# Kernel optimization log

Hardware: AMD Instinct MI355X
Metric: run time of the kernel (lower is better)

Reference implementation:

```python
import jax, jax.numpy as jnp
import numpy as np

N_HEAD = 16
NUM_GROUPS = 2


def setup_inputs() -> dict:
    key = jax.random.key(0)
    k1, k2, k3 = jax.random.split(key, 3)
    B, T, D = 4, 2048, 1024
    x = jax.random.normal(k1, (B, T, D), dtype=jnp.float32)
    W_attn = jax.random.normal(k2, (D, 3 * D), dtype=jnp.float32) * 0.02
    b_attn = jnp.zeros((3 * D,), dtype=jnp.float32)
    W_proj = jax.random.normal(k3, (D, D), dtype=jnp.float32) * 0.02
    b_proj = jnp.zeros((D,), dtype=jnp.float32)
    return {"x": x, "W_attn": W_attn, "b_attn": b_attn, "W_proj": W_proj, "b_proj": b_proj}


def _rope_tables(T, d_head):
    # thetas = 1000 ** (-2*arange(1, d/2+1)/d), repeat_interleave(2); positions start at 1
    half = d_head // 2
    thetas = 1000.0 ** (-2.0 * jnp.arange(1, half + 1, dtype=jnp.float32) / d_head)
    thetas = jnp.repeat(thetas, 2)                      # (d_head,)
    pos = jnp.arange(1, T + 1, dtype=jnp.float32)       # (T,)
    args = pos[:, None] * thetas[None, :]               # (T, d_head)
    return jnp.sin(args), jnp.cos(args)


def _apply_rope(x, sin, cos):
    # x: (B, H, T, d_head)
    x_odd = x[..., ::2]
    x_even = x[..., 1::2]
    x_sin = jnp.stack([-x_even, x_odd], axis=-1).reshape(x.shape)  # [-x1, x0, -x3, x2, ...]
    return x * cos + x_sin * sin


def reference(x, W_attn, b_attn, W_proj, b_proj):
    B, T, D = x.shape
    H = N_HEAD
    hd = D // H
    group_dim = D // NUM_GROUPS  # scale divisor; split degenerates to one group since group_dim >= hd

    qkv = x @ W_attn + b_attn                              # (B, T, 3D)
    q, k, v = jnp.split(qkv, 3, axis=-1)

    def split_heads(t):
        return t.reshape(B, T, H, hd).transpose(0, 2, 1, 3)  # (B, H, T, hd)

    q, k, v = split_heads(q), split_heads(k), split_heads(v)

    sin, cos = _rope_tables(T, hd)
    q = _apply_rope(q, sin, cos)
    k = _apply_rope(k, sin, cos)

    # NOTE: original forward never applies the causal mask (attn_mask=None) -> full softmax
    scores = jnp.einsum('bhqd,bhkd->bhqk', q, k) / jnp.sqrt(jnp.float32(group_dim))
    attn = jax.nn.softmax(scores, axis=-1)
    out = jnp.einsum('bhqk,bhkd->bhqd', attn, v)           # (B, H, T, hd)

    out = out.transpose(0, 2, 1, 3).reshape(B, T, D)       # merge heads
    return out @ W_proj + b_proj
```

## Files before the change

kernel.cpp:

```cpp
#include <hip/hip_runtime.h>
#include <hip/hip_bf16.h>
#include <stdint.h>

#define DEVI __device__ __forceinline__

using bf16x8 = __attribute__((ext_vector_type(8))) short;
using f32x4  = __attribute__((ext_vector_type(4))) float;
using f16x4  = __attribute__((ext_vector_type(4))) _Float16;
using f16x8  = __attribute__((ext_vector_type(8))) _Float16;

static constexpr int Bc = 4;
static constexpr int Tc = 2048;
static constexpr int Dc = 1024;
static constexpr int Hc = 16;
static constexpr int HDc = 64;
#define QSCALE 0.06375788883274286f

#if __has_builtin(__builtin_amdgcn_exp2f)
#define EXP2F __builtin_amdgcn_exp2f
#else
#define EXP2F exp2f
#endif

typedef const unsigned int __attribute__((address_space(1)))* gas1_t;
typedef unsigned int __attribute__((address_space(3)))* las3_t;

DEVI void gld16(const void* g, void* l)
{
    __builtin_amdgcn_global_load_lds((gas1_t)(uintptr_t)g, (las3_t)(uintptr_t)l, 16, 0, 0);
}


__global__ void f2bf_kernel(const float4* __restrict__ x, ushort4* __restrict__ y, int n4)
{
    const int base = blockIdx.x * 1024 + threadIdx.x;
#pragma unroll
    for (int u = 0; u < 4; u++) {
        const int i = base + u * 256;
        float4 v = x[i];
        union { __hip_bfloat16 h[4]; ushort4 u4; } cv;
        cv.h[0] = __float2bfloat16(v.x);
        cv.h[1] = __float2bfloat16(v.y);
        cv.h[2] = __float2bfloat16(v.z);
        cv.h[3] = __float2bfloat16(v.w);
        y[i] = cv.u4;
    }
}

__global__ void transpose_bf_kernel(const float* __restrict__ W, __hip_bfloat16* __restrict__ Wt,
                                    int K, int N)
{
    __shared__ float tile[64][65];
    const int n0 = blockIdx.x * 64, k0 = blockIdx.y * 64;
    const int tx = threadIdx.x & 15, ty = threadIdx.x >> 4;
#pragma unroll
    for (int i2 = 0; i2 < 4; i2++) {
        const int k = ty + 16 * i2;
        float4 v = *(const float4*)&W[(size_t)(k0 + k) * N + n0 + tx * 4];
        tile[tx * 4 + 0][k] = v.x;
        tile[tx * 4 + 1][k] = v.y;
        tile[tx * 4 + 2][k] = v.z;
        tile[tx * 4 + 3][k] = v.w;
    }
    __syncthreads();
#pragma unroll
    for (int i2 = 0; i2 < 4; i2++) {
        const int n = ty + 16 * i2;
        union { __hip_bfloat16 h[4]; ushort4 u4; } cv;
#pragma unroll
        for (int c = 0; c < 4; c++)
            cv.h[c] = (__hip_bfloat16)tile[n][tx * 4 + c];
        *(ushort4*)&Wt[(size_t)(n0 + n) * K + k0 + tx * 4] = cv.u4;
    }
}

__global__ void rope_tab_kernel(float* __restrict__ sinT, float* __restrict__ cosT)
{
    int i = blockIdx.x * blockDim.x + threadIdx.x;
    int t = i >> 6, dim = i & 63;
    int p = dim >> 1;
    float theta = powf(1000.f, -2.f * (float)(p + 1) / 64.f);
    float arg = (float)(t + 1) * theta;
    sinT[i] = sinf(arg);
    cosT[i] = cosf(arg);
}


template <int MODE>
__global__ __launch_bounds__(256, 2) void gemm128(
    const __hip_bfloat16* __restrict__ A, const __hip_bfloat16* __restrict__ Bt,
    const float* __restrict__ bias, int M, int N, int K,
    const float* __restrict__ sinT, const float* __restrict__ cosT,
    __hip_bfloat16* __restrict__ Qb, __hip_bfloat16* __restrict__ Kb,
    _Float16* __restrict__ Vb, float* __restrict__ Cout)
{
    __shared__ __align__(16) __hip_bfloat16 sA[2][128 * 64];
    __shared__ __align__(16) __hip_bfloat16 sB[2][128 * 64];
    const int tid = threadIdx.x;
    const int wave = tid >> 6, lane = tid & 63;
    const int qd = lane >> 4, lm = lane & 15;
    const int wm = (wave >> 1) * 64, wn = (wave & 1) * 64;
    const int tileM = blockIdx.y * 128, tileN = blockIdx.x * 128;

    const int srow = tid >> 3;
    const int socc = (tid & 7) ^ (srow & 7);

    f32x4 acc[4][4];
#pragma unroll
    for (int i = 0; i < 4; i++)
#pragma unroll
        for (int j = 0; j < 4; j++)
            acc[i][j] = (f32x4){0.f, 0.f, 0.f, 0.f};

    const __hip_bfloat16* pa = A + (size_t)(tileM + srow) * K + socc * 8;
    const __hip_bfloat16* pb = Bt + (size_t)(tileN + srow) * K + socc * 8;

    auto stageT = [&](int p, int k0) {
#pragma unroll
        for (int it = 0; it < 4; it++) {
            gld16(pa + (size_t)(it * 32) * K + k0, &sA[p][it * 2048 + wave * 512]);
            gld16(pb + (size_t)(it * 32) * K + k0, &sB[p][it * 2048 + wave * 512]);
        }
    };

    stageT(0, 0);

    const int swl = (lm & 7) << 3;
    const int nk = K / 64;
    for (int kt = 0; kt < nk; kt++) {
        const int p = kt & 1;
        if (kt + 1 < nk) {
            stageT(p ^ 1, (kt + 1) * 64);
            __builtin_amdgcn_s_waitcnt(0xF78);
        } else {
            __builtin_amdgcn_s_waitcnt(0xF70);
        }
        __builtin_amdgcn_s_barrier();

#pragma unroll
        for (int ks = 0; ks < 2; ks++) {
            bf16x8 wf[4], xf[4];
#pragma unroll
            for (int a = 0; a < 4; a++)
                wf[a] = *(const bf16x8*)&sB[p][(wn + a * 16 + lm) * 64
                                              + ((ks * 32 + qd * 8) ^ swl)];
#pragma unroll
            for (int b = 0; b < 4; b++)
                xf[b] = *(const bf16x8*)&sA[p][(wm + b * 16 + lm) * 64
                                              + ((ks * 32 + qd * 8) ^ swl)];
#pragma unroll
            for (int a = 0; a < 4; a++)
#pragma unroll
                for (int b = 0; b < 4; b++)
                    acc[a][b] = __builtin_amdgcn_mfma_f32_16x16x32_bf16(
                        wf[a], xf[b], acc[a][b], 0, 0, 0);
        }
        __builtin_amdgcn_s_barrier();
    }

    if constexpr (MODE == 0) {
        const int sec = tileN >> 10;
        const int h = ((tileN + wn) & 1023) >> 6;
#pragma unroll
        for (int a = 0; a < 4; a++) {
            const int dim0 = a * 16 + qd * 4;
            const int n0 = tileN + wn + dim0;
            const float4 bi = *(const float4*)&bias[n0];
#pragma unroll
            for (int b = 0; b < 4; b++) {
                const int m = tileM + wm + b * 16 + lm;
                const int t = m & (Tc - 1), bb = m >> 11;
                const float v0 = acc[a][b][0] + bi.x;
                const float v1 = acc[a][b][1] + bi.y;
                const float v2 = acc[a][b][2] + bi.z;
                const float v3 = acc[a][b][3] + bi.w;
                if (sec < 2) {
                    const float4 sn = *(const float4*)&sinT[t * 64 + dim0];
                    const float4 cs = *(const float4*)&cosT[t * 64 + dim0];
                    const float o0 = v0 * cs.x - v1 * sn.x;
                    const float o1 = v1 * cs.y + v0 * sn.y;
                    const float o2 = v2 * cs.z - v3 * sn.z;
                    const float o3 = v3 * cs.w + v2 * sn.w;
                    union { __hip_bfloat16 hx[4]; ushort4 u4; } cv;
                    if (sec == 0) {
                        cv.hx[0] = (__hip_bfloat16)(o0 * QSCALE);
                        cv.hx[1] = (__hip_bfloat16)(o1 * QSCALE);
                        cv.hx[2] = (__hip_bfloat16)(o2 * QSCALE);
                        cv.hx[3] = (__hip_bfloat16)(o3 * QSCALE);
                        *(ushort4*)&Qb[((size_t)(bb * Hc + h) * Tc + t) * HDc + dim0] = cv.u4;
                    } else {
                        cv.hx[0] = (__hip_bfloat16)o0;
                        cv.hx[1] = (__hip_bfloat16)o1;
                        cv.hx[2] = (__hip_bfloat16)o2;
                        cv.hx[3] = (__hip_bfloat16)o3;
                        const int dswb = dim0 ^ ((t & 7) << 3);
                        *(ushort4*)&Kb[((size_t)(bb * Hc + h) * Tc + t) * HDc + dswb] = cv.u4;
                    }
                } else {
                    const int u = t & 31;
                    const int posA = (t & ~31) + (((u & 15) >> 2) << 3)
                                     + ((u >> 4) << 2) + (u & 3);
                    const float vv[4] = {v0, v1, v2, v3};
#pragma unroll
                    for (int r = 0; r < 4; r++) {
                        const int dim = dim0 + r;
                        const int pos = posA ^ ((dim & 7) << 3);
                        Vb[((size_t)(bb * Hc + h) * HDc + dim) * Tc + pos] = (_Float16)vv[r];
                    }
                }
            }
        }
    } else {
#pragma unroll
        for (int a = 0; a < 4; a++) {
            const int n0 = tileN + wn + a * 16 + qd * 4;
            const float4 bi = *(const float4*)&bias[n0];
#pragma unroll
            for (int b = 0; b < 4; b++) {
                const int m = tileM + wm + b * 16 + lm;
                float4 o;
                o.x = acc[a][b][0] + bi.x;
                o.y = acc[a][b][1] + bi.y;
                o.z = acc[a][b][2] + bi.z;
                o.w = acc[a][b][3] + bi.w;
                *(float4*)&Cout[(size_t)m * N + n0] = o;
            }
        }
    }
}


__global__ __launch_bounds__(256, 2) void attn_kernel(
    const __hip_bfloat16* __restrict__ Qb, const __hip_bfloat16* __restrict__ Kb,
    const _Float16* __restrict__ Vh, __hip_bfloat16* __restrict__ AO)
{
    __shared__ __align__(16) __hip_bfloat16 sK[2][64 * 64];
    __shared__ __align__(16) _Float16 sV[2][64 * 64];
    const int tid = threadIdx.x, wave = tid >> 6, lane = tid & 63;
    const int qd = lane >> 4, lm = lane & 15;
    const int i = blockIdx.x;
    const int c = i & 7, j = i >> 3;
    const int bh = c + 8 * (j >> 3);
    const int qblk = j & 7;
    const int q0 = qblk * 256 + wave * 64;

    const __hip_bfloat16* Qp = Qb + (size_t)bh * Tc * HDc;
    const __hip_bfloat16* Kp = Kb + (size_t)bh * Tc * HDc;
    const _Float16* Vp = Vh + (size_t)bh * HDc * Tc;

    bf16x8 qf[4][2];
#pragma unroll
    for (int qn = 0; qn < 4; qn++)
#pragma unroll
        for (int ks = 0; ks < 2; ks++)
            qf[qn][ks] = *(const bf16x8*)(Qp + (size_t)(q0 + qn * 16 + lm) * HDc
                                          + ks * 32 + qd * 8);

    f32x4 o[4][4];
    f32x4 lsum[4];
#pragma unroll
    for (int qn = 0; qn < 4; qn++) {
#pragma unroll
        for (int cb = 0; cb < 4; cb++) o[qn][cb] = (f32x4){0.f, 0.f, 0.f, 0.f};
        lsum[qn] = (f32x4){0.f, 0.f, 0.f, 0.f};
    }
    const f16x8 one8 = {(_Float16)1.f, (_Float16)1.f, (_Float16)1.f, (_Float16)1.f,
                        (_Float16)1.f, (_Float16)1.f, (_Float16)1.f, (_Float16)1.f};

    const int swl = (lm & 7) << 3;

    auto stage = [&](int p, int k0) {
        const char* gK = (const char*)(Kp + (size_t)k0 * HDc);
#pragma unroll
        for (int jj = 0; jj < 2; jj++) {
            const int call = wave * 2 + jj;
            gld16(gK + call * 1024 + lane * 16,
                  (char*)&sK[p][0] + call * 1024 + lane * 16);
            const int dim = call * 8 + (lane >> 3);
            gld16((const char*)(Vp + (size_t)dim * Tc + k0 + (lane & 7) * 8),
                  (char*)&sV[p][0] + call * 1024 + lane * 16);
        }
    };

    stage(0, 0);

    for (int kt = 0; kt < Tc / 64; kt++) {
        const int p = kt & 1;
        if (kt < Tc / 64 - 1) {
            stage(p ^ 1, (kt + 1) * 64);
            __builtin_amdgcn_s_waitcnt(0xF74);
        } else {
            __builtin_amdgcn_s_waitcnt(0xF70);
        }
        __builtin_amdgcn_s_barrier();

        const __hip_bfloat16* bK = &sK[p][0];
        const _Float16* bV = &sV[p][0];

        f16x8 pf8[4][2];
#pragma unroll
        for (int g = 0; g < 2; g++) {
#pragma unroll
            for (int hh = 0; hh < 2; hh++) {
                const int krow = (2 * g + hh) * 16 + lm;
                bf16x8 kf0 = *(const bf16x8*)&bK[krow * 64 + ((0 + qd * 8) ^ swl)];
                bf16x8 kf1 = *(const bf16x8*)&bK[krow * 64 + ((32 + qd * 8) ^ swl)];
#pragma unroll
                for (int qn = 0; qn < 4; qn++) {
                    f32x4 s = (f32x4){0.f, 0.f, 0.f, 0.f};
                    s = __builtin_amdgcn_mfma_f32_16x16x32_bf16(kf0, qf[qn][0], s, 0, 0, 0);
                    s = __builtin_amdgcn_mfma_f32_16x16x32_bf16(kf1, qf[qn][1], s, 0, 0, 0);
                    auto lo = __builtin_amdgcn_cvt_pkrtz(EXP2F(s[0]), EXP2F(s[1]));
                    auto hi = __builtin_amdgcn_cvt_pkrtz(EXP2F(s[2]), EXP2F(s[3]));
                    pf8[qn][g][4 * hh + 0] = lo[0];
                    pf8[qn][g][4 * hh + 1] = lo[1];
                    pf8[qn][g][4 * hh + 2] = hi[0];
                    pf8[qn][g][4 * hh + 3] = hi[1];
                }
            }
        }

#pragma unroll
        for (int qn = 0; qn < 4; qn++)
#pragma unroll
            for (int g = 0; g < 2; g++)
                lsum[qn] = __builtin_amdgcn_mfma_f32_16x16x32_f16(
                    one8, pf8[qn][g], lsum[qn], 0, 0, 0);

#pragma unroll
        for (int g = 0; g < 2; g++) {
#pragma unroll
            for (int cb = 0; cb < 4; cb++) {
                f16x8 v8 = *(const f16x8*)&bV[(cb * 16 + lm) * 64
                                              + ((g * 32 + qd * 8) ^ swl)];
#pragma unroll
                for (int qn = 0; qn < 4; qn++)
                    o[qn][cb] = __builtin_amdgcn_mfma_f32_16x16x32_f16(
                        v8, pf8[qn][g], o[qn][cb], 0, 0, 0);
            }
        }
        __builtin_amdgcn_s_barrier();
    }

    const int b = bh >> 4, h = bh & 15;
#pragma unroll
    for (int qn = 0; qn < 4; qn++) {
        const float rinv = 1.f / lsum[qn][0];
        const int t = q0 + qn * 16 + lm;
#pragma unroll
        for (int cb = 0; cb < 4; cb++)
#pragma unroll
            for (int r = 0; r < 4; r++) {
                const int dim = cb * 16 + qd * 4 + r;
                AO[((size_t)b * Tc + t) * Dc + h * HDc + dim] =
                    (__hip_bfloat16)(o[qn][cb][r] * rinv);
            }
    }
}


extern "C" void kernel_launch(void* const* d_in, const int* in_sizes, int n_in,
                              void* d_out, int out_size, void* d_ws, size_t ws_size,
                              hipStream_t stream)
{
    const float* x      = (const float*)d_in[0];
    const float* W_attn = (const float*)d_in[1];
    const float* b_attn = (const float*)d_in[2];
    const float* W_proj = (const float*)d_in[3];
    const float* b_proj = (const float*)d_in[4];
    float* out = (float*)d_out;

    char* w = (char*)d_ws;
    auto alloc = [&](size_t bytes) -> char* {
        char* p = w;
        w += (bytes + 255) & ~(size_t)255;
        return p;
    };
    __hip_bfloat16* xb  = (__hip_bfloat16*)alloc((size_t)Bc * Tc * Dc * 2);
    __hip_bfloat16* Wqt = (__hip_bfloat16*)alloc((size_t)3 * Dc * Dc * 2);
    __hip_bfloat16* Wpt = (__hip_bfloat16*)alloc((size_t)Dc * Dc * 2);
    __hip_bfloat16* Qb  = (__hip_bfloat16*)alloc((size_t)Bc * Hc * Tc * HDc * 2);
    __hip_bfloat16* Kb  = (__hip_bfloat16*)alloc((size_t)Bc * Hc * Tc * HDc * 2);
    _Float16*       Vh  = (_Float16*)alloc((size_t)Bc * Hc * Tc * HDc * 2);
    __hip_bfloat16* AO  = (__hip_bfloat16*)alloc((size_t)Bc * Tc * Dc * 2);
    float* sinT = (float*)alloc((size_t)Tc * 64 * 4);
    float* cosT = (float*)alloc((size_t)Tc * 64 * 4);

    const int M = Bc * Tc;

    f2bf_kernel<<<dim3((M * Dc / 4) / 1024), dim3(256), 0, stream>>>(
        (const float4*)x, (ushort4*)xb, M * Dc / 4);
    transpose_bf_kernel<<<dim3(3 * Dc / 64, Dc / 64), dim3(256), 0, stream>>>(
        W_attn, Wqt, Dc, 3 * Dc);
    transpose_bf_kernel<<<dim3(Dc / 64, Dc / 64), dim3(256), 0, stream>>>(
        W_proj, Wpt, Dc, Dc);
    rope_tab_kernel<<<dim3(Tc * 64 / 256), dim3(256), 0, stream>>>(sinT, cosT);

    gemm128<0><<<dim3(3 * Dc / 128, M / 128), dim3(256), 0, stream>>>(
        xb, Wqt, b_attn, M, 3 * Dc, Dc, sinT, cosT, Qb, Kb, Vh, nullptr);

    attn_kernel<<<dim3(512), dim3(256), 0, stream>>>(Qb, Kb, Vh, AO);

    gemm128<1><<<dim3(Dc / 128, M / 128), dim3(256), 0, stream>>>(
        AO, Wpt, b_proj, M, Dc, Dc, nullptr, nullptr, nullptr, nullptr, nullptr, out);
}
```

Before: 267.8 us.

## Replace QKV GEMM with 256x256 tile, 8-wave kernel and interleaved staging

The QKV projection moves from a 128x128 tile with 4 waves to a 256x256 tile with 8 waves and 32 accumulators per wave. The K loop is split into four MFMA phases, and each phase issues one slice of the next tile's global-to-LDS loads with explicit waitcnt and setprio, so loads overlap compute. The aim is more operand reuse per LDS byte and better latency hiding. In exchange, the larger tile leaves fewer blocks (12x32) and raises register and LDS pressure. The output projection keeps the old 128 kernel, now specialised for that one case.

```diff
diff --git a/kernel.cpp b/kernel.cpp
--- a/kernel.cpp
+++ b/kernel.cpp
@@ -86,13 +86,188 @@
 }
 
 
-template <int MODE>
-__global__ __launch_bounds__(256, 2) void gemm128(
+__global__ __launch_bounds__(512, 2) void gemm256(
     const __hip_bfloat16* __restrict__ A, const __hip_bfloat16* __restrict__ Bt,
-    const float* __restrict__ bias, int M, int N, int K,
+    const float* __restrict__ bias, int K,
     const float* __restrict__ sinT, const float* __restrict__ cosT,
     __hip_bfloat16* __restrict__ Qb, __hip_bfloat16* __restrict__ Kb,
-    _Float16* __restrict__ Vb, float* __restrict__ Cout)
+    _Float16* __restrict__ Vb)
+{
+    __shared__ __align__(16) __hip_bfloat16 lds[2][4][128 * 64];
+    const int tid = threadIdx.x;
+    const int wave = tid >> 6, lane = tid & 63;
+    const int qd = lane >> 4, lm = lane & 15;
+    const int wm = wave >> 2, wn = wave & 3;
+    const int tileM = blockIdx.y * 256, tileN = blockIdx.x * 256;
+
+    const int srow = tid >> 3;
+    const int so = (tid & 7) ^ (srow & 7);
+
+    const __hip_bfloat16* pB0 = Bt + (size_t)(tileN + srow) * K + so * 8;
+    const __hip_bfloat16* pB1 = pB0 + (size_t)128 * K;
+    const __hip_bfloat16* pA0 = A + (size_t)(tileM + srow) * K + so * 8;
+    const __hip_bfloat16* pA1 = pA0 + (size_t)128 * K;
+
+    auto stage2 = [&](int b, int slot, const __hip_bfloat16* src) {
+        char* d = (char*)&lds[b][slot][0] + tid * 16;
+        gld16(src, d);
+        gld16(src + (size_t)64 * K, d + 8192);
+    };
+
+    f32x4 acc[4][8];
+#pragma unroll
+    for (int a = 0; a < 4; a++)
+#pragma unroll
+        for (int b = 0; b < 8; b++)
+            acc[a][b] = (f32x4){0.f, 0.f, 0.f, 0.f};
+
+    stage2(0, 0, pB0); stage2(0, 1, pB1); stage2(0, 2, pA0); stage2(0, 3, pA1);
+    stage2(1, 0, pB0 + 64); stage2(1, 1, pB1 + 64); stage2(1, 2, pA0 + 64);
+    __builtin_amdgcn_s_waitcnt(0xF76);
+    __builtin_amdgcn_s_barrier();
+
+    const int swl = (lm & 7) << 3;
+    const int o0 = (qd * 8) ^ swl, o1 = (32 + qd * 8) ^ swl;
+    const int rB0 = (wn & 1) * 64 + lm;
+    const int slB = wn >> 1;
+    const int slA = 2 + wm;
+    const int NK = K / 64;
+
+    for (int kt = 0; kt < NK; ++kt) {
+        const int buf = kt & 1;
+        const __hip_bfloat16* Bb = &lds[buf][slB][rB0 * 64];
+        const __hip_bfloat16* Ab = &lds[buf][slA][lm * 64];
+
+        bf16x8 wf[4][2], xf[4];
+#pragma unroll
+        for (int a = 0; a < 4; a++) {
+            wf[a][0] = *(const bf16x8*)(Bb + a * 1024 + o0);
+            wf[a][1] = *(const bf16x8*)(Bb + a * 1024 + o1);
+        }
+#pragma unroll
+        for (int b = 0; b < 4; b++)
+            xf[b] = *(const bf16x8*)(Ab + b * 1024 + o0);
+        if (kt + 1 < NK) stage2(buf ^ 1, 3, pA1 + (kt + 1) * 64);
+        __builtin_amdgcn_s_barrier();
+        __builtin_amdgcn_s_waitcnt(0xC07F);
+        __builtin_amdgcn_s_setprio(1);
+#pragma unroll
+        for (int a = 0; a < 4; a++)
+#pragma unroll
+            for (int b = 0; b < 4; b++)
+                acc[a][b] = __builtin_amdgcn_mfma_f32_16x16x32_bf16(
+                    wf[a][0], xf[b], acc[a][b], 0, 0, 0);
+        __builtin_amdgcn_s_setprio(0);
+        __builtin_amdgcn_s_barrier();
+
+        bf16x8 xg[4];
+#pragma unroll
+        for (int b = 0; b < 4; b++)
+            xg[b] = *(const bf16x8*)(Ab + (4 + b) * 1024 + o0);
+        if (kt + 2 < NK) stage2(buf, 0, pB0 + (kt + 2) * 64);
+        __builtin_amdgcn_s_barrier();
+        __builtin_amdgcn_s_waitcnt(0xC07F);
+        __builtin_amdgcn_s_setprio(1);
+#pragma unroll
+        for (int a = 0; a < 4; a++)
+#pragma unroll
+            for (int b = 0; b < 4; b++)
+                acc[a][4 + b] = __builtin_amdgcn_mfma_f32_16x16x32_bf16(
+                    wf[a][0], xg[b], acc[a][4 + b], 0, 0, 0);
+        __builtin_amdgcn_s_setprio(0);
+        __builtin_amdgcn_s_barrier();
+
+        bf16x8 xh[4], xi[4];
+#pragma unroll
+        for (int b = 0; b < 4; b++) {
+            xh[b] = *(const bf16x8*)(Ab + b * 1024 + o1);
+            xi[b] = *(const bf16x8*)(Ab + (4 + b) * 1024 + o1);
+        }
+        if (kt + 2 < NK) stage2(buf, 1, pB1 + (kt + 2) * 64);
+        __builtin_amdgcn_s_barrier();
+        __builtin_amdgcn_s_waitcnt(0xC07F);
+        __builtin_amdgcn_s_setprio(1);
+#pragma unroll
+        for (int a = 0; a < 4; a++)
+#pragma unroll
+            for (int b = 0; b < 4; b++)
+                acc[a][b] = __builtin_amdgcn_mfma_f32_16x16x32_bf16(
+                    wf[a][1], xh[b], acc[a][b], 0, 0, 0);
+        __builtin_amdgcn_s_setprio(0);
+        __builtin_amdgcn_s_barrier();
+
+        if (kt + 2 < NK) stage2(buf, 2, pA0 + (kt + 2) * 64);
+        __builtin_amdgcn_s_barrier();
+        __builtin_amdgcn_s_setprio(1);
+#pragma unroll
+        for (int a = 0; a < 4; a++)
+#pragma unroll
+            for (int b = 0; b < 4; b++)
+                acc[a][4 + b] = __builtin_amdgcn_mfma_f32_16x16x32_bf16(
+                    wf[a][1], xi[b], acc[a][4 + b], 0, 0, 0);
+        __builtin_amdgcn_s_setprio(0);
+        if (kt < NK - 2) __builtin_amdgcn_s_waitcnt(0xF76);
+        else             __builtin_amdgcn_s_waitcnt(0xF70);
+        __builtin_amdgcn_s_barrier();
+    }
+
+    const int sec = tileN >> 10;
+    const int h = ((tileN + wn * 64) & 1023) >> 6;
+#pragma unroll
+    for (int a = 0; a < 4; a++) {
+        const int dim0 = a * 16 + qd * 4;
+        const int n0 = tileN + wn * 64 + dim0;
+        const float4 bi = *(const float4*)&bias[n0];
+#pragma unroll
+        for (int b = 0; b < 8; b++) {
+            const int m = tileM + wm * 128 + b * 16 + lm;
+            const int t = m & (Tc - 1), bb = m >> 11;
+            const float v0 = acc[a][b][0] + bi.x;
+            const float v1 = acc[a][b][1] + bi.y;
+            const float v2 = acc[a][b][2] + bi.z;
+            const float v3 = acc[a][b][3] + bi.w;
+            if (sec < 2) {
+                const float4 sn = *(const float4*)&sinT[t * 64 + dim0];
+                const float4 cs = *(const float4*)&cosT[t * 64 + dim0];
+                const float e0 = v0 * cs.x - v1 * sn.x;
+                const float e1 = v1 * cs.y + v0 * sn.y;
+                const float e2 = v2 * cs.z - v3 * sn.z;
+                const float e3 = v3 * cs.w + v2 * sn.w;
+                union { __hip_bfloat16 hx[4]; ushort4 u4; } cv;
+                if (sec == 0) {
+                    cv.hx[0] = (__hip_bfloat16)(e0 * QSCALE);
+                    cv.hx[1] = (__hip_bfloat16)(e1 * QSCALE);
+                    cv.hx[2] = (__hip_bfloat16)(e2 * QSCALE);
+                    cv.hx[3] = (__hip_bfloat16)(e3 * QSCALE);
+                    *(ushort4*)&Qb[((size_t)(bb * Hc + h) * Tc + t) * HDc + dim0] = cv.u4;
+                } else {
+                    cv.hx[0] = (__hip_bfloat16)e0;
+                    cv.hx[1] = (__hip_bfloat16)e1;
+                    cv.hx[2] = (__hip_bfloat16)e2;
+                    cv.hx[3] = (__hip_bfloat16)e3;
+                    const int dswb = dim0 ^ ((t & 7) << 3);
+                    *(ushort4*)&Kb[((size_t)(bb * Hc + h) * Tc + t) * HDc + dswb] = cv.u4;
+                }
+            } else {
+                const int u = t & 31;
+                const int posA = (t & ~31) + (((u & 15) >> 2) << 3)
+                                 + ((u >> 4) << 2) + (u & 3);
+                const float vv[4] = {v0, v1, v2, v3};
+#pragma unroll
+                for (int r = 0; r < 4; r++) {
+                    const int dim = dim0 + r;
+                    const int pos = posA ^ ((dim & 7) << 3);
+                    Vb[((size_t)(bb * Hc + h) * HDc + dim) * Tc + pos] = (_Float16)vv[r];
+                }
+            }
+        }
+    }
+}
+
+
+__global__ __launch_bounds__(256, 2) void gemm128p(
+    const __hip_bfloat16* __restrict__ A, const __hip_bfloat16* __restrict__ Bt,
+    const float* __restrict__ bias, int N, int K, float* __restrict__ Cout)
 {
     __shared__ __align__(16) __hip_bfloat16 sA[2][128 * 64];
     __shared__ __align__(16) __hip_bfloat16 sB[2][128 * 64];
@@ -158,73 +333,19 @@
         __builtin_amdgcn_s_barrier();
     }
 
-    if constexpr (MODE == 0) {
-        const int sec = tileN >> 10;
-        const int h = ((tileN + wn) & 1023) >> 6;
-#pragma unroll
-        for (int a = 0; a < 4; a++) {
-            const int dim0 = a * 16 + qd * 4;
-            const int n0 = tileN + wn + dim0;
-            const float4 bi = *(const float4*)&bias[n0];
-#pragma unroll
-            for (int b = 0; b < 4; b++) {
-                const int m = tileM + wm + b * 16 + lm;
-                const int t = m & (Tc - 1), bb = m >> 11;
-                const float v0 = acc[a][b][0] + bi.x;
-                const float v1 = acc[a][b][1] + bi.y;
-                const float v2 = acc[a][b][2] + bi.z;
-                const float v3 = acc[a][b][3] + bi.w;
-                if (sec < 2) {
-                    const float4 sn = *(const float4*)&sinT[t * 64 + dim0];
-                    const float4 cs = *(const float4*)&cosT[t * 64 + dim0];
-                    const float o0 = v0 * cs.x - v1 * sn.x;
-                    const float o1 = v1 * cs.y + v0 * sn.y;
-                    const float o2 = v2 * cs.z - v3 * sn.z;
-                    const float o3 = v3 * cs.w + v2 * sn.w;
-                    union { __hip_bfloat16 hx[4]; ushort4 u4; } cv;
-                    if (sec == 0) {
-                        cv.hx[0] = (__hip_bfloat16)(o0 * QSCALE);
-                        cv.hx[1] = (__hip_bfloat16)(o1 * QSCALE);
-                        cv.hx[2] = (__hip_bfloat16)(o2 * QSCALE);
-                        cv.hx[3] = (__hip_bfloat16)(o3 * QSCALE);
-                        *(ushort4*)&Qb[((size_t)(bb * Hc + h) * Tc + t) * HDc + dim0] = cv.u4;
-                    } else {
-                        cv.hx[0] = (__hip_bfloat16)o0;
-                        cv.hx[1] = (__hip_bfloat16)o1;
-                        cv.hx[2] = (__hip_bfloat16)o2;
-                        cv.hx[3] = (__hip_bfloat16)o3;
-                        const int dswb = dim0 ^ ((t & 7) << 3);
-                        *(ushort4*)&Kb[((size_t)(bb * Hc + h) * Tc + t) * HDc + dswb] = cv.u4;
-                    }
-                } else {
-                    const int u = t & 31;
-                    const int posA = (t & ~31) + (((u & 15) >> 2) << 3)
-                                     + ((u >> 4) << 2) + (u & 3);
-                    const float vv[4] = {v0, v1, v2, v3};
-#pragma unroll
-                    for (int r = 0; r < 4; r++) {
-                        const int dim = dim0 + r;
-                        const int pos = posA ^ ((dim & 7) << 3);
-                        Vb[((size_t)(bb * Hc + h) * HDc + dim) * Tc + pos] = (_Float16)vv[r];
-                    }
-                }
-            }
-        }
-    } else {
-#pragma unroll
-        for (int a = 0; a < 4; a++) {
-            const int n0 = tileN + wn + a * 16 + qd * 4;
-            const float4 bi = *(const float4*)&bias[n0];
-#pragma unroll
-            for (int b = 0; b < 4; b++) {
-                const int m = tileM + wm + b * 16 + lm;
-                float4 o;
-                o.x = acc[a][b][0] + bi.x;
-                o.y = acc[a][b][1] + bi.y;
-                o.z = acc[a][b][2] + bi.z;
-                o.w = acc[a][b][3] + bi.w;
-                *(float4*)&Cout[(size_t)m * N + n0] = o;
-            }
+#pragma unroll
+    for (int a = 0; a < 4; a++) {
+        const int n0 = tileN + wn + a * 16 + qd * 4;
+        const float4 bi = *(const float4*)&bias[n0];
+#pragma unroll
+        for (int b = 0; b < 4; b++) {
+            const int m = tileM + wm + b * 16 + lm;
+            float4 o;
+            o.x = acc[a][b][0] + bi.x;
+            o.y = acc[a][b][1] + bi.y;
+            o.z = acc[a][b][2] + bi.z;
+            o.w = acc[a][b][3] + bi.w;
+            *(float4*)&Cout[(size_t)m * N + n0] = o;
         }
     }
 }
@@ -396,11 +517,11 @@
         W_proj, Wpt, Dc, Dc);
     rope_tab_kernel<<<dim3(Tc * 64 / 256), dim3(256), 0, stream>>>(sinT, cosT);
 
-    gemm128<0><<<dim3(3 * Dc / 128, M / 128), dim3(256), 0, stream>>>(
-        xb, Wqt, b_attn, M, 3 * Dc, Dc, sinT, cosT, Qb, Kb, Vh, nullptr);
+    gemm256<<<dim3(3 * Dc / 256, M / 256), dim3(512), 0, stream>>>(
+        xb, Wqt, b_attn, Dc, sinT, cosT, Qb, Kb, Vh);
 
     attn_kernel<<<dim3(512), dim3(256), 0, stream>>>(Qb, Kb, Vh, AO);
 
-    gemm128<1><<<dim3(Dc / 128, M / 128), dim3(256), 0, stream>>>(
-        AO, Wpt, b_proj, M, Dc, Dc, nullptr, nullptr, nullptr, nullptr, nullptr, out);
-}
+    gemm128p<<<dim3(Dc / 128, M / 128), dim3(256), 0, stream>>>(
+        AO, Wpt, b_proj, Dc, Dc, out);
+}
```

After: 281.7 us. 1.05x slower.
